# Performance work log

Measured on AMD Instinct MI355X. Metric: run time of the kernel, lower is better.

## Reference

```python
import jax, jax.numpy as jnp
import numpy as np

N_NODES = 100000
N_EDGES = 625000
D_IN = 128
D_HID = 256


def setup_inputs() -> dict:
    key = jax.random.key(0)
    ks = jax.random.split(key, 8)
    x = jax.random.normal(ks[0], (N_NODES, D_IN), dtype=jnp.float32)
    edge_index = jax.random.randint(ks[1], (2, N_EDGES), 0, N_NODES, dtype=jnp.int64)
    s_in = 1.0 / np.sqrt(D_IN)
    s_hid = 1.0 / np.sqrt(D_HID)
    # SAGEConv layer 0: lin_l (on aggregated neighbors, with bias) and lin_r (root)
    W_l0 = jax.random.uniform(ks[2], (D_IN, D_HID), jnp.float32, -s_in, s_in)
    W_r0 = jax.random.uniform(ks[3], (D_IN, D_HID), jnp.float32, -s_in, s_in)
    b0 = jnp.zeros((D_HID,), jnp.float32)
    # SAGEConv layer 1
    W_l1 = jax.random.uniform(ks[4], (D_HID, D_HID), jnp.float32, -s_hid, s_hid)
    W_r1 = jax.random.uniform(ks[5], (D_HID, D_HID), jnp.float32, -s_hid, s_hid)
    b1 = jnp.zeros((D_HID,), jnp.float32)
    return {"x": x, "edge_index": edge_index,
            "W_l0": W_l0, "W_r0": W_r0, "b0": b0,
            "W_l1": W_l1, "W_r1": W_r1, "b1": b1}


def _sage_conv(x, src, dst, W_l, W_r, b):
    """PyG SAGEConv with mean aggregation: lin_l(mean_{j in N(i)} x_j) + lin_r(x_i)."""
    n = x.shape[0]
    msg = x[src]  # [E, d] gather of source-node features
    agg_sum = jax.ops.segment_sum(msg, dst, num_segments=n)  # scatter-add to targets
    cnt = jax.ops.segment_sum(jnp.ones_like(dst, dtype=x.dtype), dst, num_segments=n)
    agg = agg_sum / jnp.maximum(cnt, 1.0)[:, None]  # mean over neighbors
    return agg @ W_l + b + x @ W_r


def reference(x, edge_index, W_l0, W_r0, b0, W_l1, W_r1, b1):
    src, dst = edge_index[0], edge_index[1]
    h = _sage_conv(x, src, dst, W_l0, W_r0, b0)
    h = jax.nn.relu(h)  # dropout is identity at inference
    h = _sage_conv(h, src, dst, W_l1, W_r1, b1)
    h = jax.nn.relu(h)
    return h
```

## Files before the change

kernel.cpp:

```cpp
#include <hip/hip_runtime.h>


constexpr int NN   = 100000;
constexpr int NE   = 625000;
constexpr int DIN  = 128;
constexpr int DHID = 256;
constexpr int NB   = (NN + 255) / 256;
constexpr int CONV_BLKS = NN * DIN / 8 / 256;

using short8 = __attribute__((ext_vector_type(8))) short;
using f32x4  = __attribute__((ext_vector_type(4))) float;

__device__ __forceinline__ float bf2f(unsigned int u) {
    return __uint_as_float(u << 16);
}
__device__ __forceinline__ unsigned short f2b(float f) {
    unsigned int u = __float_as_uint(f);
    unsigned int r = (u + 0x7fffu + ((u >> 16) & 1u)) >> 16;
    return (unsigned short)r;
}
__device__ __forceinline__ unsigned int pack2(float lo, float hi) {
    return (unsigned int)f2b(lo) | ((unsigned int)f2b(hi) << 16);
}
__device__ __forceinline__ void gload16(const void* g, void* lds) {
    __builtin_amdgcn_global_load_lds(
        (const __attribute__((address_space(1))) void*)g,
        (__attribute__((address_space(3))) void*)lds, 16, 0, 0);
}

__global__ __launch_bounds__(256) void zero_kernel(int* __restrict__ p, int n)
{
    int t = blockIdx.x * 256 + threadIdx.x;
    if (t < n) p[t] = 0;
}

__global__ __launch_bounds__(256) void hist_kernel(const int* __restrict__ dst,
                                                   int* __restrict__ hist)
{
    int t = blockIdx.x * 256 + threadIdx.x;
    if (t < NE) atomicAdd(&hist[dst[t]], 1);
}

__global__ __launch_bounds__(256) void chunk_sum_kernel(const int* __restrict__ hist,
                                                        int* __restrict__ bsum)
{
    __shared__ int s[256];
    int i = blockIdx.x * 256 + threadIdx.x;
    s[threadIdx.x] = (i < NN) ? hist[i] : 0;
    __syncthreads();
    for (int off = 128; off > 0; off >>= 1) {
        if (threadIdx.x < off) s[threadIdx.x] += s[threadIdx.x + off];
        __syncthreads();
    }
    if (threadIdx.x == 0) bsum[blockIdx.x] = s[0];
}

__global__ __launch_bounds__(512) void scan_bsum_kernel(const int* __restrict__ bsum,
                                                        int* __restrict__ bpre)
{
    __shared__ int s[512];
    int t = threadIdx.x;
    int v = (t < NB) ? bsum[t] : 0;
    s[t] = v;
    __syncthreads();
    for (int off = 1; off < 512; off <<= 1) {
        int u = (t >= off) ? s[t - off] : 0;
        __syncthreads();
        s[t] += u;
        __syncthreads();
    }
    if (t < NB) bpre[t] = s[t] - v;
}

__global__ __launch_bounds__(256) void scatter_offs_kernel(const int* __restrict__ hist,
                                                           const int* __restrict__ bpre,
                                                           int* __restrict__ offs,
                                                           int* __restrict__ cursor)
{
    __shared__ int s[256];
    int t = threadIdx.x;
    int i = blockIdx.x * 256 + t;
    int v = (i < NN) ? hist[i] : 0;
    s[t] = v;
    __syncthreads();
    for (int off = 1; off < 256; off <<= 1) {
        int u = (t >= off) ? s[t - off] : 0;
        __syncthreads();
        s[t] += u;
        __syncthreads();
    }
    int excl = s[t] - v + bpre[blockIdx.x];
    if (i < NN) {
        offs[i]   = excl;
        cursor[i] = excl;
    }
    if (i == NN - 1) offs[NN] = NE;
}

__global__ __launch_bounds__(256) void perm_kernel(const int* __restrict__ src,
                                                   const int* __restrict__ dst,
                                                   int* __restrict__ cursor,
                                                   int* __restrict__ perm)
{
    int t = blockIdx.x * 256 + threadIdx.x;
    if (t < NE) {
        int p = atomicAdd(&cursor[dst[t]], 1);
        perm[p] = src[t];
    }
}

__global__ __launch_bounds__(256) void prep_all_kernel(
    const float* __restrict__ x, unsigned short* __restrict__ xb,
    const float* __restrict__ Wl0, const float* __restrict__ Wr0,
    unsigned short* __restrict__ WT0,
    const float* __restrict__ Wl1, const float* __restrict__ Wr1,
    unsigned short* __restrict__ WT1)
{
    int b = blockIdx.x;
    if (b < CONV_BLKS) {
        int t = b * 256 + threadIdx.x;
        float4 v0 = reinterpret_cast<const float4*>(x)[t * 2 + 0];
        float4 v1 = reinterpret_cast<const float4*>(x)[t * 2 + 1];
        uint4 o;
        o.x = pack2(v0.x, v0.y); o.y = pack2(v0.z, v0.w);
        o.z = pack2(v1.x, v1.y); o.w = pack2(v1.z, v1.w);
        reinterpret_cast<uint4*>(xb)[t] = o;
    } else if (b < CONV_BLKS + 256) {
        int t = (b - CONV_BLKS) * 256 + threadIdx.x;
        int n = t >> 8, k = t & 255;
        float v = (k < DIN) ? Wl0[(size_t)k * DHID + n]
                            : Wr0[(size_t)(k - DIN) * DHID + n];
        WT0[t] = f2b(v);
    } else {
        int t = (b - CONV_BLKS - 256) * 256 + threadIdx.x;
        int n = t >> 9, k = t & 511;
        float v = (k < DHID) ? Wl1[(size_t)k * DHID + n]
                             : Wr1[(size_t)(k - DHID) * DHID + n];
        WT1[t] = f2b(v);
    }
}

template <int D>
__global__ __launch_bounds__(256) void gather_mean_kernel(
    const int* __restrict__ offs, const int* __restrict__ perm,
    const unsigned short* __restrict__ feat, unsigned short* __restrict__ agg)
{
    const int w    = (blockIdx.x * 256 + threadIdx.x) >> 6;
    const int lane = threadIdx.x & 63;
    if (w >= NN) return;
    const int beg = offs[w], end = offs[w + 1];
    const int deg = end - beg;
    const float sc = 1.0f / (float)(deg > 1 ? deg : 1);

    if constexpr (D == 256) {
        const uint2* base = reinterpret_cast<const uint2*>(feat);
        float a0[4] = {}, a1[4] = {}, a2[4] = {}, a3[4] = {};
        for (int e0 = 0; e0 < deg; e0 += 64) {
            const int chunk = min(deg - e0, 64);
            int pv = (lane < chunk) ? perm[beg + e0 + lane] : 0;
            int i = chunk & 3;
            if (i > 0) {
                int s = __builtin_amdgcn_readlane(pv, 0);
                uint2 v = base[(size_t)s * 64 + lane];
                a1[0] += bf2f(v.x & 0xffffu); a1[1] += bf2f(v.x >> 16);
                a1[2] += bf2f(v.y & 0xffffu); a1[3] += bf2f(v.y >> 16);
            }
            if (i > 1) {
                int s = __builtin_amdgcn_readlane(pv, 1);
                uint2 v = base[(size_t)s * 64 + lane];
                a2[0] += bf2f(v.x & 0xffffu); a2[1] += bf2f(v.x >> 16);
                a2[2] += bf2f(v.y & 0xffffu); a2[3] += bf2f(v.y >> 16);
            }
            if (i > 2) {
                int s = __builtin_amdgcn_readlane(pv, 2);
                uint2 v = base[(size_t)s * 64 + lane];
                a3[0] += bf2f(v.x & 0xffffu); a3[1] += bf2f(v.x >> 16);
                a3[2] += bf2f(v.y & 0xffffu); a3[3] += bf2f(v.y >> 16);
            }
            for (; i + 4 <= chunk; i += 4) {
                int s0 = __builtin_amdgcn_readlane(pv, i + 0);
                int s1 = __builtin_amdgcn_readlane(pv, i + 1);
                int s2 = __builtin_amdgcn_readlane(pv, i + 2);
                int s3 = __builtin_amdgcn_readlane(pv, i + 3);
                uint2 v0 = base[(size_t)s0 * 64 + lane];
                uint2 v1 = base[(size_t)s1 * 64 + lane];
                uint2 v2 = base[(size_t)s2 * 64 + lane];
                uint2 v3 = base[(size_t)s3 * 64 + lane];
                a0[0] += bf2f(v0.x & 0xffffu); a0[1] += bf2f(v0.x >> 16);
                a0[2] += bf2f(v0.y & 0xffffu); a0[3] += bf2f(v0.y >> 16);
                a1[0] += bf2f(v1.x & 0xffffu); a1[1] += bf2f(v1.x >> 16);
                a1[2] += bf2f(v1.y & 0xffffu); a1[3] += bf2f(v1.y >> 16);
                a2[0] += bf2f(v2.x & 0xffffu); a2[1] += bf2f(v2.x >> 16);
                a2[2] += bf2f(v2.y & 0xffffu); a2[3] += bf2f(v2.y >> 16);
                a3[0] += bf2f(v3.x & 0xffffu); a3[1] += bf2f(v3.x >> 16);
                a3[2] += bf2f(v3.y & 0xffffu); a3[3] += bf2f(v3.y >> 16);
            }
        }
        float r0 = (a0[0] + a1[0]) + (a2[0] + a3[0]);
        float r1 = (a0[1] + a1[1]) + (a2[1] + a3[1]);
        float r2 = (a0[2] + a1[2]) + (a2[2] + a3[2]);
        float r3 = (a0[3] + a1[3]) + (a2[3] + a3[3]);
        uint2 o;
        o.x = pack2(r0 * sc, r1 * sc);
        o.y = pack2(r2 * sc, r3 * sc);
        reinterpret_cast<uint2*>(agg)[(size_t)w * 64 + lane] = o;
    } else {
        const unsigned int* base = reinterpret_cast<const unsigned int*>(feat);
        float a0[2] = {}, a1[2] = {}, a2[2] = {}, a3[2] = {};
        for (int e0 = 0; e0 < deg; e0 += 64) {
            const int chunk = min(deg - e0, 64);
            int pv = (lane < chunk) ? perm[beg + e0 + lane] : 0;
            int i = chunk & 3;
            if (i > 0) {
                int s = __builtin_amdgcn_readlane(pv, 0);
                unsigned int v = base[(size_t)s * 64 + lane];
                a1[0] += bf2f(v & 0xffffu); a1[1] += bf2f(v >> 16);
            }
            if (i > 1) {
                int s = __builtin_amdgcn_readlane(pv, 1);
                unsigned int v = base[(size_t)s * 64 + lane];
                a2[0] += bf2f(v & 0xffffu); a2[1] += bf2f(v >> 16);
            }
            if (i > 2) {
                int s = __builtin_amdgcn_readlane(pv, 2);
                unsigned int v = base[(size_t)s * 64 + lane];
                a3[0] += bf2f(v & 0xffffu); a3[1] += bf2f(v >> 16);
            }
            for (; i + 4 <= chunk; i += 4) {
                int s0 = __builtin_amdgcn_readlane(pv, i + 0);
                int s1 = __builtin_amdgcn_readlane(pv, i + 1);
                int s2 = __builtin_amdgcn_readlane(pv, i + 2);
                int s3 = __builtin_amdgcn_readlane(pv, i + 3);
                unsigned int v0 = base[(size_t)s0 * 64 + lane];
                unsigned int v1 = base[(size_t)s1 * 64 + lane];
                unsigned int v2 = base[(size_t)s2 * 64 + lane];
                unsigned int v3 = base[(size_t)s3 * 64 + lane];
                a0[0] += bf2f(v0 & 0xffffu); a0[1] += bf2f(v0 >> 16);
                a1[0] += bf2f(v1 & 0xffffu); a1[1] += bf2f(v1 >> 16);
                a2[0] += bf2f(v2 & 0xffffu); a2[1] += bf2f(v2 >> 16);
                a3[0] += bf2f(v3 & 0xffffu); a3[1] += bf2f(v3 >> 16);
            }
        }
        float r0 = (a0[0] + a1[0]) + (a2[0] + a3[0]);
        float r1 = (a0[1] + a1[1]) + (a2[1] + a3[1]);
        reinterpret_cast<unsigned int*>(agg)[(size_t)w * 64 + lane] = pack2(r0 * sc, r1 * sc);
    }
}

template <int KP, bool WF, bool WB>
__global__ __launch_bounds__(256) void sage_mfma_gemm(
    const unsigned short* __restrict__ Aagg,
    const unsigned short* __restrict__ Axr,
    const unsigned short* __restrict__ WT,
    const float* __restrict__ bias,
    float* __restrict__ outf,
    unsigned short* __restrict__ outb,
    int M)
{
    __shared__ __align__(16) unsigned short As[2][128 * 32];
    __shared__ __align__(16) unsigned short Bs[2][128 * 32];

    const int t   = threadIdx.x;
    const int l   = t & 63;
    const int wid = t >> 6;
    const int wr  = wid >> 1, wc = wid & 1;
    const int m0  = blockIdx.x * 128;
    const int c0  = blockIdx.y * 128;

    const int rin = l >> 2;
    const int csw = (l & 3) ^ ((l >> 3) & 3);
    const int ch0 = wid * 2, ch1 = ch0 + 1;

    int arow0 = m0 + ch0 * 16 + rin; if (arow0 >= M) arow0 = M - 1;
    int arow1 = m0 + ch1 * 16 + rin; if (arow1 >= M) arow1 = M - 1;
    const int brow0 = c0 + ch0 * 16 + rin;
    const int brow1 = c0 + ch1 * 16 + rin;

    constexpr int K2 = 2 * KP;
    constexpr int KT = K2 / 32;

    auto stage = [&](int buf, int kt) {
        const int kb = kt * 32;
        const unsigned short* Asrc;
        int kk;
        if (kb < KP) { Asrc = Aagg; kk = kb; }
        else         { Asrc = Axr;  kk = kb - KP; }
        gload16(Asrc + (size_t)arow0 * KP + kk + csw * 8, As[buf] + ch0 * 512);
        gload16(Asrc + (size_t)arow1 * KP + kk + csw * 8, As[buf] + ch1 * 512);
        gload16(WT + (size_t)brow0 * K2 + kb + csw * 8, Bs[buf] + ch0 * 512);
        gload16(WT + (size_t)brow1 * K2 + kb + csw * 8, Bs[buf] + ch1 * 512);
    };

    const int fr  = l & 15;
    const int swz = ((l >> 4) ^ ((l >> 1) & 3)) * 8;
    const int aOff = (wr * 64 + fr) * 32 + swz;
    const int bOff = (wc * 64 + fr) * 32 + swz;

    f32x4 acc[4][4] = {};

    stage(0, 0);

    #pragma unroll 2
    for (int kt = 0; kt < KT; ++kt) {
        const int cur = kt & 1;
        if (kt + 1 < KT) {
            stage(cur ^ 1, kt + 1);
            asm volatile("s_waitcnt vmcnt(4)" ::: "memory");
        } else {
            asm volatile("s_waitcnt vmcnt(0)" ::: "memory");
        }
        __builtin_amdgcn_s_barrier();
        __builtin_amdgcn_sched_barrier(0);

        const unsigned short* Ard = As[cur] + aOff;
        const unsigned short* Brd = Bs[cur] + bOff;
        short8 af[4], bf[4];
        #pragma unroll
        for (int i = 0; i < 4; ++i)
            af[i] = *reinterpret_cast<const short8*>(Ard + i * 512);
        #pragma unroll
        for (int i = 0; i < 4; ++i)
            bf[i] = *reinterpret_cast<const short8*>(Brd + i * 512);
        #pragma unroll
        for (int i = 0; i < 4; ++i)
            #pragma unroll
            for (int j = 0; j < 4; ++j)
                acc[i][j] = __builtin_amdgcn_mfma_f32_16x16x32_bf16(
                    af[i], bf[j], acc[i][j], 0, 0, 0);

        asm volatile("s_waitcnt lgkmcnt(0)" ::: "memory");
        __builtin_amdgcn_s_barrier();
        __builtin_amdgcn_sched_barrier(0);
    }

    const int rq = (l >> 4) * 4;
    #pragma unroll
    for (int fn = 0; fn < 4; ++fn) {
        const int col = c0 + wc * 64 + fn * 16 + fr;
        const float bb = bias[col];
        #pragma unroll
        for (int fm = 0; fm < 4; ++fm) {
            const int rbase = m0 + wr * 64 + fm * 16 + rq;
            #pragma unroll
            for (int j = 0; j < 4; ++j) {
                const int r = rbase + j;
                if (r < M) {
                    float v = fmaxf(acc[fm][fn][j] + bb, 0.f);
                    if (WF) outf[(size_t)r * DHID + col] = v;
                    if (WB) outb[(size_t)r * DHID + col] = f2b(v);
                }
            }
        }
    }
}

extern "C" void kernel_launch(void* const* d_in, const int* in_sizes, int n_in,
                              void* d_out, int out_size, void* d_ws, size_t ws_size,
                              hipStream_t stream)
{
    const float* x   = (const float*)d_in[0];
    const int*   ei  = (const int*)d_in[1];
    const int*   src = ei;
    const int*   dst = ei + NE;
    const float* Wl0 = (const float*)d_in[2];
    const float* Wr0 = (const float*)d_in[3];
    const float* b0  = (const float*)d_in[4];
    const float* Wl1 = (const float*)d_in[5];
    const float* Wr1 = (const float*)d_in[6];
    const float* b1  = (const float*)d_in[7];
    float* out = (float*)d_out;

    char* ws = (char*)d_ws;
    int*            hist   = (int*)(ws);
    int*            offs   = (int*)(ws + 400384);
    int*            perm   = (int*)(ws + 801024);
    int*            bsum   = (int*)(ws + 3301376);
    int*            bpre   = (int*)(ws + 3305472);
    int*            cursor = (int*)(ws + 3309568);
    unsigned short* WT0    = (unsigned short*)(ws + 3709952);
    unsigned short* WT1    = (unsigned short*)(ws + 3841024);
    unsigned short* xb     = (unsigned short*)(ws + 4103168);
    unsigned short* h0b    = (unsigned short*)(ws + 29703168);
    unsigned short* aggb   = (unsigned short*)(ws + 80903168);

    zero_kernel<<<(NN + 255) / 256, 256, 0, stream>>>(hist, NN);
    hist_kernel<<<(NE + 255) / 256, 256, 0, stream>>>(dst, hist);
    chunk_sum_kernel<<<NB, 256, 0, stream>>>(hist, bsum);
    scan_bsum_kernel<<<1, 512, 0, stream>>>(bsum, bpre);
    scatter_offs_kernel<<<NB, 256, 0, stream>>>(hist, bpre, offs, cursor);
    perm_kernel<<<(NE + 255) / 256, 256, 0, stream>>>(src, dst, cursor, perm);

    prep_all_kernel<<<CONV_BLKS + 256 + 512, 256, 0, stream>>>(
        x, xb, Wl0, Wr0, WT0, Wl1, Wr1, WT1);

    constexpr int NWBLK = (NN * 64) / 256;
    dim3 ggrid((NN + 127) / 128, DHID / 128);

    gather_mean_kernel<DIN><<<NWBLK, 256, 0, stream>>>(offs, perm, xb, aggb);
    sage_mfma_gemm<DIN, false, true><<<ggrid, 256, 0, stream>>>(
        aggb, xb, WT0, b0, nullptr, h0b, NN);

    gather_mean_kernel<DHID><<<NWBLK, 256, 0, stream>>>(offs, perm, h0b, aggb);
    sage_mfma_gemm<DHID, true, false><<<ggrid, 256, 0, stream>>>(
        aggb, h0b, WT1, b1, out, nullptr, NN);
}
```

Measured before the change: 298.5 us.

## Widen GEMM tile to full 256 output columns with 512 threads and triple buffering

```diff
diff --git a/kernel.cpp b/kernel.cpp
--- a/kernel.cpp
+++ b/kernel.cpp
@@ -248,7 +248,7 @@
 }
 
 template <int KP, bool WF, bool WB>
-__global__ __launch_bounds__(256) void sage_mfma_gemm(
+__global__ __launch_bounds__(512) void sage_mfma_gemm(
     const unsigned short* __restrict__ Aagg,
     const unsigned short* __restrict__ Axr,
     const unsigned short* __restrict__ WT,
@@ -257,38 +257,44 @@
     unsigned short* __restrict__ outb,
     int M)
 {
-    __shared__ __align__(16) unsigned short As[2][128 * 32];
-    __shared__ __align__(16) unsigned short Bs[2][128 * 32];
+    __shared__ __align__(16) unsigned short As[3 * 4096];
+    __shared__ __align__(16) unsigned short Bs[3 * 8192];
 
     const int t   = threadIdx.x;
     const int l   = t & 63;
     const int wid = t >> 6;
-    const int wr  = wid >> 1, wc = wid & 1;
+    const int wr  = wid >> 2;
+    const int wc  = wid & 3;
     const int m0  = blockIdx.x * 128;
-    const int c0  = blockIdx.y * 128;
 
     const int rin = l >> 2;
     const int csw = (l & 3) ^ ((l >> 3) & 3);
-    const int ch0 = wid * 2, ch1 = ch0 + 1;
-
-    int arow0 = m0 + ch0 * 16 + rin; if (arow0 >= M) arow0 = M - 1;
-    int arow1 = m0 + ch1 * 16 + rin; if (arow1 >= M) arow1 = M - 1;
-    const int brow0 = c0 + ch0 * 16 + rin;
-    const int brow1 = c0 + ch1 * 16 + rin;
+
+    const int sc0 = wid * 3, sc1 = sc0 + 1, sc2 = sc0 + 2;
 
     constexpr int K2 = 2 * KP;
     constexpr int KT = K2 / 32;
 
+    auto stageChunk = [&](int buf, int kt, int ch) {
+        const int kb = kt * 32;
+        if (ch < 8) {
+            const unsigned short* Asrc;
+            int kk;
+            if (kb < KP) { Asrc = Aagg; kk = kb; }
+            else         { Asrc = Axr;  kk = kb - KP; }
+            int row = m0 + ch * 16 + rin; if (row >= M) row = M - 1;
+            gload16(Asrc + (size_t)row * KP + kk + csw * 8,
+                    As + buf * 4096 + ch * 512);
+        } else {
+            int row = (ch - 8) * 16 + rin;
+            gload16(WT + (size_t)row * K2 + kb + csw * 8,
+                    Bs + buf * 8192 + (ch - 8) * 512);
+        }
+    };
     auto stage = [&](int buf, int kt) {
-        const int kb = kt * 32;
-        const unsigned short* Asrc;
-        int kk;
-        if (kb < KP) { Asrc = Aagg; kk = kb; }
-        else         { Asrc = Axr;  kk = kb - KP; }
-        gload16(Asrc + (size_t)arow0 * KP + kk + csw * 8, As[buf] + ch0 * 512);
-        gload16(Asrc + (size_t)arow1 * KP + kk + csw * 8, As[buf] + ch1 * 512);
-        gload16(WT + (size_t)brow0 * K2 + kb + csw * 8, Bs[buf] + ch0 * 512);
-        gload16(WT + (size_t)brow1 * K2 + kb + csw * 8, Bs[buf] + ch1 * 512);
+        stageChunk(buf, kt, sc0);
+        stageChunk(buf, kt, sc1);
+        stageChunk(buf, kt, sc2);
     };
 
     const int fr  = l & 15;
@@ -299,21 +305,24 @@
     f32x4 acc[4][4] = {};
 
     stage(0, 0);
-
-    #pragma unroll 2
+    stage(1, 1);
+
+    int cur = 0;
     for (int kt = 0; kt < KT; ++kt) {
-        const int cur = kt & 1;
-        if (kt + 1 < KT) {
-            stage(cur ^ 1, kt + 1);
-            asm volatile("s_waitcnt vmcnt(4)" ::: "memory");
+        if (kt + 2 < KT) {
+            int nb = cur + 2; if (nb >= 3) nb -= 3;
+            stage(nb, kt + 2);
+            asm volatile("s_waitcnt vmcnt(6)" ::: "memory");
+        } else if (kt + 1 < KT) {
+            asm volatile("s_waitcnt vmcnt(3)" ::: "memory");
         } else {
             asm volatile("s_waitcnt vmcnt(0)" ::: "memory");
         }
         __builtin_amdgcn_s_barrier();
         __builtin_amdgcn_sched_barrier(0);
 
-        const unsigned short* Ard = As[cur] + aOff;
-        const unsigned short* Brd = Bs[cur] + bOff;
+        const unsigned short* Ard = As + cur * 4096 + aOff;
+        const unsigned short* Brd = Bs + cur * 8192 + bOff;
         short8 af[4], bf[4];
         #pragma unroll
         for (int i = 0; i < 4; ++i)
@@ -331,12 +340,13 @@
         asm volatile("s_waitcnt lgkmcnt(0)" ::: "memory");
         __builtin_amdgcn_s_barrier();
         __builtin_amdgcn_sched_barrier(0);
+        cur = (cur == 2) ? 0 : cur + 1;
     }
 
     const int rq = (l >> 4) * 4;
     #pragma unroll
     for (int fn = 0; fn < 4; ++fn) {
-        const int col = c0 + wc * 64 + fn * 16 + fr;
+        const int col = wc * 64 + fn * 16 + fr;
         const float bb = bias[col];
         #pragma unroll
         for (int fm = 0; fm < 4; ++fm) {
@@ -394,13 +404,13 @@
         x, xb, Wl0, Wr0, WT0, Wl1, Wr1, WT1);
 
     constexpr int NWBLK = (NN * 64) / 256;
-    dim3 ggrid((NN + 127) / 128, DHID / 128);
+    const int GEMM_BLKS = (NN + 127) / 128;
 
     gather_mean_kernel<DIN><<<NWBLK, 256, 0, stream>>>(offs, perm, xb, aggb);
-    sage_mfma_gemm<DIN, false, true><<<ggrid, 256, 0, stream>>>(
+    sage_mfma_gemm<DIN, false, true><<<GEMM_BLKS, 512, 0, stream>>>(
         aggb, xb, WT0, b0, nullptr, h0b, NN);
 
     gather_mean_kernel<DHID><<<NWBLK, 256, 0, stream>>>(offs, perm, h0b, aggb);
-    sage_mfma_gemm<DHID, true, false><<<ggrid, 256, 0, stream>>>(
+    sage_mfma_gemm<DHID, true, false><<<GEMM_BLKS, 512, 0, stream>>>(
         aggb, h0b, WT1, b1, out, nullptr, NN);
 }
```

Measured after the change: 273.7 us. 8.3% less time.
